# Performance work log

Measured on AMD Instinct MI355X. Metric: run time of the kernel, lower is better.

The kernel has to match this reference:

```python
import jax, jax.numpy as jnp
import numpy as np

B, N, D, H = 4, 2048, 1024, 16
HD = D // H
SCALE = D ** -0.5  # NOTE: original scales by dimension**-0.5 (not head_dim**-0.5)


def setup_inputs() -> dict:
    key = jax.random.key(0)
    k1, k2, k3 = jax.random.split(key, 3)
    x = jax.random.normal(k1, (B, N, D), dtype=jnp.float32)
    w_qkv = jax.random.normal(k2, (D, 3 * D), dtype=jnp.float32) * (D ** -0.5)
    w_proj = jax.random.normal(k3, (D, D), dtype=jnp.float32) * (D ** -0.5)
    b_proj = jnp.zeros((D,), dtype=jnp.float32)
    return {"x": x, "w_qkv": w_qkv, "w_proj": w_proj, "b_proj": b_proj}


def reference(x, w_qkv, w_proj, b_proj):
    # qkv projection: [B,N,3D] -> split into q,k,v each [B,H,N,HD]
    qkv = x @ w_qkv
    qkv = qkv.reshape(B, N, 3, H, HD).transpose(2, 0, 3, 1, 4)  # [3,B,H,N,HD]
    q, k, v = qkv[0], qkv[1], qkv[2]
    scores = jnp.einsum('bhid,bhjd->bhij', q, k) * SCALE
    attn = jax.nn.softmax(scores, axis=-1)
    out = jnp.einsum('bhij,bhjd->bhid', attn, v)  # [B,H,N,HD]
    out = out.transpose(0, 2, 1, 3).reshape(B, N, D)
    return out @ w_proj + b_proj
```

## Files before the change

### kernel.cpp

```cpp
#include <hip/hip_runtime.h>
#include <stdint.h>

#define Bdim 4
#define Nseq 2048
#define Dmod 1024
#define Hn   16
#define HD   64
#define SCALE 0.03125f
#define L2E   1.44269504089f

typedef __attribute__((ext_vector_type(8))) short short8;
typedef __attribute__((ext_vector_type(8))) unsigned short ushort8;
typedef __attribute__((ext_vector_type(4))) float f32x4;
typedef __attribute__((ext_vector_type(16))) float f32x16;

static __device__ __forceinline__ unsigned short f2bf(float f) {
    union { float f; uint32_t u; } v; v.f = f;
    uint32_t r = (v.u + 0x7FFFu + ((v.u >> 16) & 1u)) >> 16;
    return (unsigned short)r;
}

__global__ __launch_bounds__(256) void cast_x_kernel(const float* __restrict__ in,
                                                     unsigned short* __restrict__ out, int n4) {
    int i = blockIdx.x * blockDim.x + threadIdx.x;
    int stride = gridDim.x * blockDim.x;
    for (; i < n4; i += stride) {
        float4 v = reinterpret_cast<const float4*>(in)[i];
        ushort4 o;
        o.x = f2bf(v.x); o.y = f2bf(v.y); o.z = f2bf(v.z); o.w = f2bf(v.w);
        reinterpret_cast<ushort4*>(out)[i] = o;
    }
}

__global__ void transpose_cast_kernel(const float* __restrict__ in,
                                      unsigned short* __restrict__ out, int R, int C) {
    __shared__ unsigned short t[32][33];
    int c0 = blockIdx.x * 32, r0 = blockIdx.y * 32;
    int tx = threadIdx.x, ty = threadIdx.y;
#pragma unroll
    for (int i = 0; i < 4; ++i)
        t[ty + i*8][tx] = f2bf(in[(size_t)(r0 + ty + i*8) * C + c0 + tx]);
    __syncthreads();
#pragma unroll
    for (int i = 0; i < 4; ++i)
        out[(size_t)(c0 + ty + i*8) * R + r0 + tx] = t[tx][ty + i*8];
}

template<bool OUT_BF16, bool BIAS>
__global__ __launch_bounds__(256) void gemm_bt_kernel(const unsigned short* __restrict__ A,
                                                      const unsigned short* __restrict__ Bt,
                                                      void* __restrict__ Cv,
                                                      const float* __restrict__ bias,
                                                      int M, int N, int K) {
    __shared__ unsigned short Al[128][72];
    __shared__ unsigned short Bl[128][72];
    int tid = threadIdx.x;
    int lane = tid & 63, wv = tid >> 6;
    int wr = (wv >> 1) * 64, wc = (wv & 1) * 64;
    int lr = lane & 15, lg = lane >> 4;
    int lk = lg * 8;
    int m0 = blockIdx.y * 128, n0 = blockIdx.x * 128;
    int srow = tid >> 1, scol = (tid & 1) * 32;

    f32x4 acc[4][4];
#pragma unroll
    for (int i = 0; i < 4; ++i)
#pragma unroll
        for (int j = 0; j < 4; ++j) acc[i][j] = (f32x4)0.f;

    for (int k0 = 0; k0 < K; k0 += 64) {
        __syncthreads();
        const ushort8* ag = reinterpret_cast<const ushort8*>(A + (size_t)(m0 + srow) * K + k0 + scol);
        const ushort8* bg = reinterpret_cast<const ushort8*>(Bt + (size_t)(n0 + srow) * K + k0 + scol);
#pragma unroll
        for (int j = 0; j < 4; ++j) {
            *reinterpret_cast<ushort8*>(&Al[srow][scol + j*8]) = ag[j];
            *reinterpret_cast<ushort8*>(&Bl[srow][scol + j*8]) = bg[j];
        }
        __syncthreads();
#pragma unroll
        for (int ks = 0; ks < 2; ++ks) {
            short8 a[4], b[4];
#pragma unroll
            for (int mi = 0; mi < 4; ++mi)
                a[mi] = *reinterpret_cast<const short8*>(&Al[wr + mi*16 + lr][ks*32 + lk]);
#pragma unroll
            for (int nj = 0; nj < 4; ++nj)
                b[nj] = *reinterpret_cast<const short8*>(&Bl[wc + nj*16 + lr][ks*32 + lk]);
#pragma unroll
            for (int mi = 0; mi < 4; ++mi)
#pragma unroll
                for (int nj = 0; nj < 4; ++nj)
                    acc[mi][nj] = __builtin_amdgcn_mfma_f32_16x16x32_bf16(a[mi], b[nj], acc[mi][nj], 0, 0, 0);
        }
    }
#pragma unroll
    for (int mi = 0; mi < 4; ++mi) {
#pragma unroll
        for (int nj = 0; nj < 4; ++nj) {
            int r = m0 + wr + mi*16 + lg*4;
            int c = n0 + wc + nj*16 + lr;
            float bv = BIAS ? bias[c] : 0.f;
#pragma unroll
            for (int i = 0; i < 4; ++i) {
                float v = acc[mi][nj][i] + bv;
                if (OUT_BF16)
                    reinterpret_cast<unsigned short*>(Cv)[(size_t)(r + i) * N + c] = f2bf(v);
                else
                    reinterpret_cast<float*>(Cv)[(size_t)(r + i) * N + c] = v;
            }
        }
    }
}

__global__ __launch_bounds__(256) void transpose_v_kernel(const unsigned short* __restrict__ qkv,
                                                          unsigned short* __restrict__ vT) {
    __shared__ unsigned short t[64][68];
    int bh = blockIdx.y, b = bh >> 4, h = bh & 15;
    int j0 = blockIdx.x * 64;
    int tid = threadIdx.x;
#pragma unroll
    for (int p = 0; p < 4; ++p) {
        int e = p * 256 + tid;
        int jj = e >> 4;
        int d4 = (e & 15) * 4;
        const unsigned short* src = qkv + (size_t)(b*Nseq + j0 + jj) * 3072 + 2048 + h*64 + d4;
        ushort4 v = *reinterpret_cast<const ushort4*>(src);
        *reinterpret_cast<ushort4*>(&t[jj][d4]) = v;
    }
    __syncthreads();
#pragma unroll
    for (int p = 0; p < 4; ++p) {
        int e = p * 256 + tid;
        int d = e >> 4;
        int j4 = (e & 15) * 4;
        ushort4 v;
        v.x = t[j4 + 0][d]; v.y = t[j4 + 1][d]; v.z = t[j4 + 2][d]; v.w = t[j4 + 3][d];
        *reinterpret_cast<ushort4*>(vT + ((size_t)bh * 64 + d) * Nseq + j0 + j4) = v;
    }
}

__global__ __launch_bounds__(256) void attn_kernel(const unsigned short* __restrict__ qkv,
                                                   const unsigned short* __restrict__ vT,
                                                   unsigned short* __restrict__ attn_o) {
    __shared__ unsigned short Kl[64 * 64];
    __shared__ unsigned short Vl[64 * 64];
    __shared__ unsigned short Pl[4 * 32 * 64];

    int w = blockIdx.x;
    int lid = (w & 7) * 128 + (w >> 3);
    int bh = lid >> 4, qb = lid & 15;
    int b = bh >> 4, h = bh & 15;

    int tid = threadIdx.x, lane = tid & 63, wv = tid >> 6;
    int lr = lane & 31, hi = lane >> 5;
    int q0 = qb * 128 + wv * 32;

    short8 qf[4];
    {
        const unsigned short* qrow = qkv + (size_t)(b * Nseq + q0 + lr) * 3072 + h * 64 + hi * 8;
#pragma unroll
        for (int ks = 0; ks < 4; ++ks)
            qf[ks] = *reinterpret_cast<const short8*>(qrow + ks * 16);
    }

    float mrun = -1e30f, lrun = 0.f;
    f32x16 oacc0 = (f32x16)0.f, oacc1 = (f32x16)0.f;

    int sr = tid >> 2;
    int sc = (tid & 3) * 32;
    const unsigned short* kg = qkv + (size_t)(b * Nseq + sr) * 3072 + 1024 + h * 64 + sc / 2;
    const unsigned short* vg = vT + ((size_t)(bh * 64 + sr)) * Nseq + sc / 2;
    int swz0 = sr * 128 + ((sc) ^ ((sr & 7) << 4));
    int swz1 = sr * 128 + ((sc + 16) ^ ((sr & 7) << 4));
    int rswz = (lr & 7) << 4;
    char* PlW = (char*)Pl + wv * 4096 + lr * 128;

    for (int jt = 0; jt < Nseq; jt += 64) {
        ushort8 k0 = *reinterpret_cast<const ushort8*>(kg + (size_t)jt * 3072);
        ushort8 k1 = *reinterpret_cast<const ushort8*>(kg + (size_t)jt * 3072 + 8);
        ushort8 v0 = *reinterpret_cast<const ushort8*>(vg + jt);
        ushort8 v1 = *reinterpret_cast<const ushort8*>(vg + jt + 8);
        __syncthreads();
        *reinterpret_cast<ushort8*>((char*)Kl + swz0) = k0;
        *reinterpret_cast<ushort8*>((char*)Kl + swz1) = k1;
        *reinterpret_cast<ushort8*>((char*)Vl + swz0) = v0;
        *reinterpret_cast<ushort8*>((char*)Vl + swz1) = v1;
        __syncthreads();

        f32x16 s0 = (f32x16)0.f, s1 = (f32x16)0.f;
#pragma unroll
        for (int ks = 0; ks < 4; ++ks) {
            int cb = ks * 32 + hi * 16;
            short8 kf0 = *reinterpret_cast<const short8*>((char*)Kl + lr * 128 + (cb ^ rswz));
            short8 kf1 = *reinterpret_cast<const short8*>((char*)Kl + (lr + 32) * 128 + (cb ^ rswz));
            s0 = __builtin_amdgcn_mfma_f32_32x32x16_bf16(kf0, qf[ks], s0, 0, 0, 0);
            s1 = __builtin_amdgcn_mfma_f32_32x32x16_bf16(kf1, qf[ks], s1, 0, 0, 0);
        }

        float mloc = s0[0];
#pragma unroll
        for (int i = 1; i < 16; ++i) mloc = fmaxf(mloc, s0[i]);
#pragma unroll
        for (int i = 0; i < 16; ++i) mloc = fmaxf(mloc, s1[i]);
        mloc = fmaxf(mloc, __shfl_xor(mloc, 32));
        float mnew = fmaxf(mrun, mloc * SCALE);
        float fac = __builtin_amdgcn_exp2f((mrun - mnew) * L2E);
        const float c1 = SCALE * L2E;
        float c0 = -mnew * L2E;
        float ps = 0.f;
        float p0[16], p1[16];
#pragma unroll
        for (int i = 0; i < 16; ++i) { p0[i] = __builtin_amdgcn_exp2f(fmaf(s0[i], c1, c0)); ps += p0[i]; }
#pragma unroll
        for (int i = 0; i < 16; ++i) { p1[i] = __builtin_amdgcn_exp2f(fmaf(s1[i], c1, c0)); ps += p1[i]; }
        ps += __shfl_xor(ps, 32);
        lrun = lrun * fac + ps;
        mrun = mnew;
#pragma unroll
        for (int i = 0; i < 16; ++i) { oacc0[i] *= fac; oacc1[i] *= fac; }

        uint32_t W[16];
#pragma unroll
        for (int m = 0; m < 8; ++m)
            W[m] = (uint32_t)f2bf(p0[2*m]) | ((uint32_t)f2bf(p0[2*m+1]) << 16);
#pragma unroll
        for (int m = 0; m < 8; ++m)
            W[8+m] = (uint32_t)f2bf(p1[2*m]) | ((uint32_t)f2bf(p1[2*m+1]) << 16);
#pragma unroll
        for (int t = 0; t < 8; ++t) {
            uint64_t val = (uint64_t)W[2*t] | ((uint64_t)W[2*t+1] << 32);
            *reinterpret_cast<uint64_t*>(PlW + ((16*t + 8*hi) ^ rswz)) = val;
        }

#pragma unroll
        for (int ks4 = 0; ks4 < 4; ++ks4) {
            int cb = ks4 * 32 + hi * 16;
            short8 pf  = *reinterpret_cast<const short8*>(PlW + (cb ^ rswz));
            short8 vf0 = *reinterpret_cast<const short8*>((char*)Vl + lr * 128 + (cb ^ rswz));
            short8 vf1 = *reinterpret_cast<const short8*>((char*)Vl + (lr + 32) * 128 + (cb ^ rswz));
            oacc0 = __builtin_amdgcn_mfma_f32_32x32x16_bf16(vf0, pf, oacc0, 0, 0, 0);
            oacc1 = __builtin_amdgcn_mfma_f32_32x32x16_bf16(vf1, pf, oacc1, 0, 0, 0);
        }
    }

    float inv = 1.f / lrun;
    unsigned short* orow = attn_o + (size_t)(b * Nseq + q0 + lr) * Dmod + h * 64;
#pragma unroll
    for (int db = 0; db < 2; ++db)
#pragma unroll
        for (int g = 0; g < 4; ++g) {
            ushort4 o4;
            float v0 = (db ? oacc1[4*g+0] : oacc0[4*g+0]) * inv;
            float v1 = (db ? oacc1[4*g+1] : oacc0[4*g+1]) * inv;
            float v2 = (db ? oacc1[4*g+2] : oacc0[4*g+2]) * inv;
            float v3 = (db ? oacc1[4*g+3] : oacc0[4*g+3]) * inv;
            o4.x = f2bf(v0); o4.y = f2bf(v1); o4.z = f2bf(v2); o4.w = f2bf(v3);
            int d = db * 32 + 8 * g + 4 * hi;
            *reinterpret_cast<ushort4*>(orow + d) = o4;
        }
}

extern "C" void kernel_launch(void* const* d_in, const int* in_sizes, int n_in,
                              void* d_out, int out_size, void* d_ws, size_t ws_size,
                              hipStream_t stream) {
    const float* x      = (const float*)d_in[0];
    const float* w_qkv  = (const float*)d_in[1];
    const float* w_proj = (const float*)d_in[2];
    const float* b_proj = (const float*)d_in[3];
    float* out = (float*)d_out;
    char* ws = (char*)d_ws;

    unsigned short* qkv    = (unsigned short*)(ws);
    unsigned short* vT     = (unsigned short*)(ws + 50331648);
    unsigned short* xb     = (unsigned short*)(ws + 67108864);
    unsigned short* attn_o = xb;
    unsigned short* wqkvT  = (unsigned short*)(ws + 83886080);
    unsigned short* wprojT = (unsigned short*)(ws + 90177536);

    cast_x_kernel<<<2048, 256, 0, stream>>>(x, xb, (Bdim*Nseq*Dmod)/4);
    transpose_cast_kernel<<<dim3(3072/32, 1024/32), dim3(32, 8), 0, stream>>>(w_qkv, wqkvT, 1024, 3072);
    transpose_cast_kernel<<<dim3(1024/32, 1024/32), dim3(32, 8), 0, stream>>>(w_proj, wprojT, 1024, 1024);
    gemm_bt_kernel<true, false><<<dim3(3072/128, 8192/128), 256, 0, stream>>>(
        xb, wqkvT, qkv, nullptr, Bdim*Nseq, 3*Dmod, Dmod);
    transpose_v_kernel<<<dim3(Nseq/64, Bdim*Hn), 256, 0, stream>>>(qkv, vT);
    attn_kernel<<<1024, 256, 0, stream>>>(qkv, vT, attn_o);
    gemm_bt_kernel<false, true><<<dim3(1024/128, 8192/128), 256, 0, stream>>>(
        attn_o, wprojT, out, b_proj, Bdim*Nseq, Dmod, Dmod);
}
```

Measured before the change: 255.6 us.

## Use direct global-to-LDS loads in GEMM and prefetch K/V tiles in attention

Result: no change. 250.9 us (-1.8%).

```diff
diff --git a/kernel.cpp b/kernel.cpp
--- a/kernel.cpp
+++ b/kernel.cpp
@@ -13,6 +13,13 @@
 typedef __attribute__((ext_vector_type(8))) unsigned short ushort8;
 typedef __attribute__((ext_vector_type(4))) float f32x4;
 typedef __attribute__((ext_vector_type(16))) float f32x16;
+
+typedef __attribute__((address_space(3))) uint32_t lds_u32;
+typedef __attribute__((address_space(1))) const uint32_t glob_u32;
+
+static __device__ __forceinline__ void gload_lds16(const unsigned short* g, unsigned short* l) {
+    __builtin_amdgcn_global_load_lds((glob_u32*)(const void*)g, (lds_u32*)(void*)l, 16, 0, 0);
+}
 
 static __device__ __forceinline__ unsigned short f2bf(float f) {
     union { float f; uint32_t u; } v; v.f = f;
@@ -52,15 +59,20 @@
                                                       void* __restrict__ Cv,
                                                       const float* __restrict__ bias,
                                                       int M, int N, int K) {
-    __shared__ unsigned short Al[128][72];
-    __shared__ unsigned short Bl[128][72];
+    __shared__ unsigned short Al[128 * 64];
+    __shared__ unsigned short Bl[128 * 64];
     int tid = threadIdx.x;
     int lane = tid & 63, wv = tid >> 6;
     int wr = (wv >> 1) * 64, wc = (wv & 1) * 64;
-    int lr = lane & 15, lg = lane >> 4;
-    int lk = lg * 8;
+    int lr = lane & 15, lg = lane >> 4, lk = lg * 8;
     int m0 = blockIdx.y * 128, n0 = blockIdx.x * 128;
-    int srow = tid >> 1, scol = (tid & 1) * 32;
+
+    int srow = wv * 8 + (lane >> 3);
+    int scol = (lane & 7) * 8;
+    const unsigned short* ag = A  + (size_t)(m0 + srow) * K + scol;
+    const unsigned short* bg = Bt + (size_t)(n0 + srow) * K + scol;
+    unsigned short* la = Al + wv * 512;
+    unsigned short* lb = Bl + wv * 512;
 
     f32x4 acc[4][4];
 #pragma unroll
@@ -70,12 +82,10 @@
 
     for (int k0 = 0; k0 < K; k0 += 64) {
         __syncthreads();
-        const ushort8* ag = reinterpret_cast<const ushort8*>(A + (size_t)(m0 + srow) * K + k0 + scol);
-        const ushort8* bg = reinterpret_cast<const ushort8*>(Bt + (size_t)(n0 + srow) * K + k0 + scol);
-#pragma unroll
-        for (int j = 0; j < 4; ++j) {
-            *reinterpret_cast<ushort8*>(&Al[srow][scol + j*8]) = ag[j];
-            *reinterpret_cast<ushort8*>(&Bl[srow][scol + j*8]) = bg[j];
+#pragma unroll
+        for (int i = 0; i < 4; ++i) {
+            gload_lds16(ag + (size_t)i * 32 * K + k0, la + i * 2048);
+            gload_lds16(bg + (size_t)i * 32 * K + k0, lb + i * 2048);
         }
         __syncthreads();
 #pragma unroll
@@ -83,10 +93,10 @@
             short8 a[4], b[4];
 #pragma unroll
             for (int mi = 0; mi < 4; ++mi)
-                a[mi] = *reinterpret_cast<const short8*>(&Al[wr + mi*16 + lr][ks*32 + lk]);
+                a[mi] = *reinterpret_cast<const short8*>(Al + (wr + mi*16 + lr) * 64 + ks*32 + lk);
 #pragma unroll
             for (int nj = 0; nj < 4; ++nj)
-                b[nj] = *reinterpret_cast<const short8*>(&Bl[wc + nj*16 + lr][ks*32 + lk]);
+                b[nj] = *reinterpret_cast<const short8*>(Bl + (wc + nj*16 + lr) * 64 + ks*32 + lk);
 #pragma unroll
             for (int mi = 0; mi < 4; ++mi)
 #pragma unroll
@@ -176,19 +186,28 @@
     int rswz = (lr & 7) << 4;
     char* PlW = (char*)Pl + wv * 4096 + lr * 128;
 
+    ushort8 k0r = *reinterpret_cast<const ushort8*>(kg);
+    ushort8 k1r = *reinterpret_cast<const ushort8*>(kg + 8);
+    ushort8 v0r = *reinterpret_cast<const ushort8*>(vg);
+    ushort8 v1r = *reinterpret_cast<const ushort8*>(vg + 8);
+
     for (int jt = 0; jt < Nseq; jt += 64) {
-        ushort8 k0 = *reinterpret_cast<const ushort8*>(kg + (size_t)jt * 3072);
-        ushort8 k1 = *reinterpret_cast<const ushort8*>(kg + (size_t)jt * 3072 + 8);
-        ushort8 v0 = *reinterpret_cast<const ushort8*>(vg + jt);
-        ushort8 v1 = *reinterpret_cast<const ushort8*>(vg + jt + 8);
         __syncthreads();
-        *reinterpret_cast<ushort8*>((char*)Kl + swz0) = k0;
-        *reinterpret_cast<ushort8*>((char*)Kl + swz1) = k1;
-        *reinterpret_cast<ushort8*>((char*)Vl + swz0) = v0;
-        *reinterpret_cast<ushort8*>((char*)Vl + swz1) = v1;
+        *reinterpret_cast<ushort8*>((char*)Kl + swz0) = k0r;
+        *reinterpret_cast<ushort8*>((char*)Kl + swz1) = k1r;
+        *reinterpret_cast<ushort8*>((char*)Vl + swz0) = v0r;
+        *reinterpret_cast<ushort8*>((char*)Vl + swz1) = v1r;
+        int jn = jt + 64;
+        if (jn < Nseq) {
+            k0r = *reinterpret_cast<const ushort8*>(kg + (size_t)jn * 3072);
+            k1r = *reinterpret_cast<const ushort8*>(kg + (size_t)jn * 3072 + 8);
+            v0r = *reinterpret_cast<const ushort8*>(vg + jn);
+            v1r = *reinterpret_cast<const ushort8*>(vg + jn + 8);
+        }
         __syncthreads();
 
         f32x16 s0 = (f32x16)0.f, s1 = (f32x16)0.f;
+        __builtin_amdgcn_s_setprio(1);
 #pragma unroll
         for (int ks = 0; ks < 4; ++ks) {
             int cb = ks * 32 + hi * 16;
@@ -197,24 +216,33 @@
             s0 = __builtin_amdgcn_mfma_f32_32x32x16_bf16(kf0, qf[ks], s0, 0, 0, 0);
             s1 = __builtin_amdgcn_mfma_f32_32x32x16_bf16(kf1, qf[ks], s1, 0, 0, 0);
         }
-
-        float mloc = s0[0];
-#pragma unroll
-        for (int i = 1; i < 16; ++i) mloc = fmaxf(mloc, s0[i]);
-#pragma unroll
-        for (int i = 0; i < 16; ++i) mloc = fmaxf(mloc, s1[i]);
-        mloc = fmaxf(mloc, __shfl_xor(mloc, 32));
+        __builtin_amdgcn_s_setprio(0);
+
+        float t[16];
+#pragma unroll
+        for (int i = 0; i < 16; ++i) t[i] = fmaxf(s0[i], s1[i]);
+#pragma unroll
+        for (int st = 8; st > 0; st >>= 1)
+#pragma unroll
+            for (int i = 0; i < st; ++i) t[i] = fmaxf(t[i], t[i + st]);
+        float mloc = fmaxf(t[0], __shfl_xor(t[0], 32));
         float mnew = fmaxf(mrun, mloc * SCALE);
         float fac = __builtin_amdgcn_exp2f((mrun - mnew) * L2E);
         const float c1 = SCALE * L2E;
         float c0 = -mnew * L2E;
-        float ps = 0.f;
         float p0[16], p1[16];
 #pragma unroll
-        for (int i = 0; i < 16; ++i) { p0[i] = __builtin_amdgcn_exp2f(fmaf(s0[i], c1, c0)); ps += p0[i]; }
-#pragma unroll
-        for (int i = 0; i < 16; ++i) { p1[i] = __builtin_amdgcn_exp2f(fmaf(s1[i], c1, c0)); ps += p1[i]; }
-        ps += __shfl_xor(ps, 32);
+        for (int i = 0; i < 16; ++i) p0[i] = __builtin_amdgcn_exp2f(fmaf(s0[i], c1, c0));
+#pragma unroll
+        for (int i = 0; i < 16; ++i) p1[i] = __builtin_amdgcn_exp2f(fmaf(s1[i], c1, c0));
+        float a[16];
+#pragma unroll
+        for (int i = 0; i < 16; ++i) a[i] = p0[i] + p1[i];
+#pragma unroll
+        for (int st = 8; st > 0; st >>= 1)
+#pragma unroll
+            for (int i = 0; i < st; ++i) a[i] = a[i] + a[i + st];
+        float ps = a[0] + __shfl_xor(a[0], 32);
         lrun = lrun * fac + ps;
         mrun = mnew;
 #pragma unroll
@@ -222,17 +250,17 @@
 
         uint32_t W[16];
 #pragma unroll
-        for (int m = 0; m < 8; ++m)
-            W[m] = (uint32_t)f2bf(p0[2*m]) | ((uint32_t)f2bf(p0[2*m+1]) << 16);
-#pragma unroll
-        for (int m = 0; m < 8; ++m)
-            W[8+m] = (uint32_t)f2bf(p1[2*m]) | ((uint32_t)f2bf(p1[2*m+1]) << 16);
-#pragma unroll
-        for (int t = 0; t < 8; ++t) {
-            uint64_t val = (uint64_t)W[2*t] | ((uint64_t)W[2*t+1] << 32);
-            *reinterpret_cast<uint64_t*>(PlW + ((16*t + 8*hi) ^ rswz)) = val;
-        }
-
+        for (int m = 0; m < 8; ++m) {
+            asm("v_cvt_pk_bf16_f32 %0, %1, %2" : "=v"(W[m])   : "v"(p0[2*m]), "v"(p0[2*m+1]));
+            asm("v_cvt_pk_bf16_f32 %0, %1, %2" : "=v"(W[8+m]) : "v"(p1[2*m]), "v"(p1[2*m+1]));
+        }
+#pragma unroll
+        for (int tt = 0; tt < 8; ++tt) {
+            uint64_t val = (uint64_t)W[2*tt] | ((uint64_t)W[2*tt+1] << 32);
+            *reinterpret_cast<uint64_t*>(PlW + ((16*tt + 8*hi) ^ rswz)) = val;
+        }
+
+        __builtin_amdgcn_s_setprio(1);
 #pragma unroll
         for (int ks4 = 0; ks4 < 4; ++ks4) {
             int cb = ks4 * 32 + hi * 16;
@@ -242,6 +270,7 @@
             oacc0 = __builtin_amdgcn_mfma_f32_32x32x16_bf16(vf0, pf, oacc0, 0, 0, 0);
             oacc1 = __builtin_amdgcn_mfma_f32_32x32x16_bf16(vf1, pf, oacc1, 0, 0, 0);
         }
+        __builtin_amdgcn_s_setprio(0);
     }
 
     float inv = 1.f / lrun;
```
